# Kernel optimization log

Hardware: AMD Instinct MI355X
Metric: run time of the kernel (lower is better)

The kernel has to match this reference:

```python
import jax, jax.numpy as jnp
import numpy as np

B, T, D_MODEL = 2, 8192, 2048
H, H_KV, D_HEAD = 16, 8, 128
M_LAND, RANK = 64, 64
N_ITER = 6
STD = 0.02


def setup_inputs() -> dict:
    key = jax.random.key(0)
    ks = jax.random.split(key, 7)
    return {
        "x": jax.random.normal(ks[0], (B, T, D_MODEL), jnp.float32),
        "Wq": jax.random.normal(ks[1], (D_MODEL, H * D_HEAD), jnp.float32) * STD,
        "Wk": jax.random.normal(ks[2], (D_MODEL, H_KV * D_HEAD), jnp.float32) * STD,
        "Wv": jax.random.normal(ks[3], (D_MODEL, H_KV * D_HEAD), jnp.float32) * STD,
        "Wo": jax.random.normal(ks[4], (H * D_HEAD, D_MODEL), jnp.float32) * STD,
        "Wkp1": jax.random.normal(ks[5], (D_HEAD, RANK), jnp.float32) * STD,
        "Wkp2": jax.random.normal(ks[6], (RANK, D_HEAD), jnp.float32) * STD,
    }


def _iterative_pinv(A, n_iter=N_ITER):
    # A: (B, H, m, m); Schulz iteration Z <- 2Z - Z A Z
    norm_1 = jnp.max(jnp.sum(jnp.abs(A), axis=-2), axis=-1)
    norm_inf = jnp.max(jnp.sum(jnp.abs(A), axis=-1), axis=-1)
    v = 1.0 / jnp.clip(norm_1 * norm_inf, 1e-7)
    Z = jnp.swapaxes(A, -1, -2) * v[..., None, None]
    for _ in range(n_iter):
        Z = 2.0 * Z - Z @ A @ Z
    return Z


def reference(x, Wq, Wk, Wv, Wo, Wkp1, Wkp2):
    n_rep = H // H_KV
    # projections -> (B, H, T, d)
    q = (x @ Wq).reshape(B, T, H, D_HEAD).transpose(0, 2, 1, 3)
    k = (x @ Wk).reshape(B, T, H_KV, D_HEAD).transpose(0, 2, 1, 3)
    v = (x @ Wv).reshape(B, T, H_KV, D_HEAD).transpose(0, 2, 1, 3)
    k = jnp.repeat(k, n_rep, axis=1)  # GQA repeat_kv
    v = jnp.repeat(v, n_rep, axis=1)

    m = min(M_LAND, T)
    scale = 1.0 / np.sqrt(D_HEAD).astype(np.float32)
    stride = max(T // m, 1)
    idx = jnp.arange(0, T, stride)[:m]
    q_land = q[:, :, idx, :]
    k_land = k[:, :, idx, :]
    kernel_proj = lambda z: z + jax.nn.silu(z @ Wkp1) @ Wkp2
    q_land = kernel_proj(q_land)
    k_land = kernel_proj(k_land)

    K_qm = jax.nn.softmax(jnp.einsum('bhtd,bhmd->bhtm', q, k_land) * scale, axis=-1)
    K_mm = jax.nn.softmax(jnp.einsum('bhmd,bhnd->bhmn', q_land, k_land) * scale, axis=-1)
    K_mk = jax.nn.softmax(jnp.einsum('bhmd,bhtd->bhmt', q_land, k) * scale, axis=-1)
    K_mm_inv = _iterative_pinv(K_mm)

    # associativity-reordered (same math, avoids dense (T,T) intermediate)
    out = K_qm @ (K_mm_inv @ (K_mk @ v))  # (B, H, T, d)
    out = out.transpose(0, 2, 1, 3).reshape(B, T, H * D_HEAD)
    return out @ Wo
```

## Files before the change

### kernel.cpp

```cpp
#include <hip/hip_runtime.h>


#define B_ 2
#define T_ 8192
#define DM 2048
#define H_ 16
#define DH 128
#define NIT 6

typedef unsigned short u16;
typedef __attribute__((ext_vector_type(8))) short bf16x8;
typedef __attribute__((ext_vector_type(4))) float f32x4;
typedef __attribute__((ext_vector_type(4))) unsigned short u16x4;

__device__ __forceinline__ u16 f2bf(float f) {
    unsigned u = __float_as_uint(f);
    u += 0x7FFFu + ((u >> 16) & 1u);
    return (u16)(u >> 16);
}

__device__ __forceinline__ void async16(const void* g, void* l) {
    __builtin_amdgcn_global_load_lds((const __attribute__((address_space(1))) void*)g,
                                     (__attribute__((address_space(3))) void*)l,
                                     16, 0, 0);
}

__global__ void cvt_x_kernel(const float* __restrict__ x, u16* __restrict__ xb, int n4) {
    int i = blockIdx.x * blockDim.x + threadIdx.x;
    int stride = gridDim.x * blockDim.x;
    for (; i < n4; i += stride) {
        float4 v = ((const float4*)x)[i];
        u16x4 o;
        o.x = f2bf(v.x); o.y = f2bf(v.y); o.z = f2bf(v.z); o.w = f2bf(v.w);
        ((u16x4*)xb)[i] = o;
    }
}

__global__ void tconv_kernel(const float* __restrict__ src, u16* __restrict__ dst, int R, int C) {
    __shared__ float tl[32][33];
    int c0 = blockIdx.x * 32, r0 = blockIdx.y * 32;
    int tx = threadIdx.x, ty = threadIdx.y;
    #pragma unroll
    for (int i = ty; i < 32; i += 8)
        tl[i][tx] = src[(size_t)(r0 + i) * C + c0 + tx];
    __syncthreads();
    #pragma unroll
    for (int i = ty; i < 32; i += 8)
        dst[(size_t)(c0 + i) * R + r0 + tx] = f2bf(tl[tx][i]);
}

__global__ void tv_kernel(const u16* __restrict__ v, u16* __restrict__ vT) {
    int bg = blockIdx.z;
    const u16* src = v + (size_t)(bg >> 3) * T_ * 1024 + (bg & 7) * DH;
    u16* dst = vT + (size_t)bg * DH * T_;
    __shared__ u16 tl[32][33];
    int t0 = blockIdx.x * 32, d0 = blockIdx.y * 32;
    int tx = threadIdx.x, ty = threadIdx.y;
    #pragma unroll
    for (int i = ty; i < 32; i += 8)
        tl[i][tx] = src[(size_t)(t0 + i) * 1024 + d0 + tx];
    __syncthreads();
    #pragma unroll
    for (int i = ty; i < 32; i += 8)
        dst[(size_t)(d0 + i) * T_ + t0 + tx] = tl[tx][i];
}

template<int MODE>
__global__ __launch_bounds__(256) void gemm_bt_kernel(
    const u16* __restrict__ A, const u16* __restrict__ Bt,
    u16* __restrict__ oq, u16* __restrict__ ok, u16* __restrict__ ov,
    float* __restrict__ of, int M, int N, int K)
{
    __shared__ u16 la[128 * 32];
    __shared__ u16 lb[128 * 32];
    const int tid = threadIdx.x;
    const int lane = tid & 63;
    const int w = tid >> 6;
    const int wr = w >> 1, wc = w & 1;
    const int fr = lane & 15, fg = lane >> 4;
    const long row0 = (long)blockIdx.y * 128;
    const long col0 = (long)blockIdx.x * 128;

    const u16* ga = A + (row0 + (tid >> 2)) * (long)K + (tid & 3) * 8;
    const u16* gb = Bt + (col0 + (tid >> 2)) * (long)K + (tid & 3) * 8;
    char* la_b = (char*)la + w * 1024;
    char* lb_b = (char*)lb + w * 1024;

    const u16* lap = la + (wr * 64 + fr) * 32 + fg * 8;
    const u16* lbp = lb + (wc * 64 + fr) * 32 + fg * 8;

    f32x4 acc[4][4] = {};

    for (int k0 = 0; k0 < K; k0 += 32) {
        __syncthreads();
        async16(ga + k0, la_b);
        async16(ga + k0 + 64 * (long)K, la_b + 4096);
        async16(gb + k0, lb_b);
        async16(gb + k0 + 64 * (long)K, lb_b + 4096);
        __syncthreads();
        bf16x8 af[4], bfv[4];
        #pragma unroll
        for (int i = 0; i < 4; ++i) af[i] = *(const bf16x8*)(lap + i * 16 * 32);
        #pragma unroll
        for (int j = 0; j < 4; ++j) bfv[j] = *(const bf16x8*)(lbp + j * 16 * 32);
        #pragma unroll
        for (int i = 0; i < 4; ++i)
            #pragma unroll
            for (int j = 0; j < 4; ++j)
                acc[i][j] = __builtin_amdgcn_mfma_f32_16x16x32_bf16(af[i], bfv[j], acc[i][j], 0, 0, 0);
    }

    const long rbase = row0 + wr * 64 + fg * 4;
    const int nbase = (int)col0 + wc * 64 + fr;
    #pragma unroll
    for (int i = 0; i < 4; ++i)
        #pragma unroll
        for (int j = 0; j < 4; ++j)
            #pragma unroll
            for (int r = 0; r < 4; ++r) {
                long rg = rbase + i * 16 + r;
                int nn = nbase + j * 16;
                float val = acc[i][j][r];
                if (MODE == 0) {
                    u16 o = f2bf(val);
                    if (nn < 2048)      oq[rg * 2048 + nn] = o;
                    else if (nn < 3072) ok[rg * 1024 + (nn - 2048)] = o;
                    else                ov[rg * 1024 + (nn - 3072)] = o;
                } else {
                    of[rg * 2048 + nn] = val;
                }
            }
}

__global__ __launch_bounds__(256) void land_gemm_kernel(
    const float* __restrict__ x, const float* __restrict__ Wq,
    const float* __restrict__ Wk, float* __restrict__ land_raw)
{
    __shared__ float xs[128][36];
    __shared__ float ws[32][132];
    const int tid = threadIdx.x;
    const int n0 = blockIdx.x * 128;
    const int tm0 = (tid >> 4) * 8, tn0 = (tid & 15) * 8;
    float accr[8][8] = {};

    for (int it = 0; it < 8; ++it) {
        const int k0 = blockIdx.y * 256 + it * 32;
        __syncthreads();
        for (int idx = tid * 4; idx < 4096; idx += 1024) {
            int r = idx >> 5, c = idx & 31;
            *(float4*)&xs[r][c] =
                *(const float4*)&x[((size_t)(r >> 6) * T_ + (r & 63) * 128) * DM + k0 + c];
        }
        if (n0 < 2048) {
            for (int idx = tid * 4; idx < 4096; idx += 1024) {
                int k = idx >> 7, c = idx & 127;
                *(float4*)&ws[k][c] = *(const float4*)&Wq[(size_t)(k0 + k) * 2048 + n0 + c];
            }
        } else {
            for (int idx = tid * 4; idx < 4096; idx += 1024) {
                int k = idx >> 7, c = idx & 127;
                *(float4*)&ws[k][c] = *(const float4*)&Wk[(size_t)(k0 + k) * 1024 + (n0 - 2048) + c];
            }
        }
        __syncthreads();
        for (int k = 0; k < 32; ++k) {
            float a[8];
            #pragma unroll
            for (int i = 0; i < 8; ++i) a[i] = xs[tm0 + i][k];
            f32x4 b0 = *(const f32x4*)&ws[k][tn0];
            f32x4 b1 = *(const f32x4*)&ws[k][tn0 + 4];
            #pragma unroll
            for (int i = 0; i < 8; ++i) {
                accr[i][0] += a[i] * b0[0]; accr[i][1] += a[i] * b0[1];
                accr[i][2] += a[i] * b0[2]; accr[i][3] += a[i] * b0[3];
                accr[i][4] += a[i] * b1[0]; accr[i][5] += a[i] * b1[1];
                accr[i][6] += a[i] * b1[2]; accr[i][7] += a[i] * b1[3];
            }
        }
    }
    for (int i = 0; i < 8; ++i)
        for (int j = 0; j < 8; ++j)
            atomicAdd(&land_raw[(size_t)(tm0 + i) * 3072 + n0 + tn0 + j], accr[i][j]);
}

__global__ void proj_kernel(const float* __restrict__ land_raw,
    const float* __restrict__ Wkp1, const float* __restrict__ Wkp2,
    float* __restrict__ qlf, float* __restrict__ klf,
    u16* __restrict__ qlb, u16* __restrict__ klb)
{
    const int bid = blockIdx.x;
    const int type = bid & 1;
    const int m = (bid >> 1) & 63;
    const int bh = bid >> 7;
    const int b = bh >> 4, h = bh & 15;
    const int lane = threadIdx.x;
    const int lm = b * 64 + m;
    const float* src = (type == 0)
        ? land_raw + (size_t)lm * 3072 + h * 128
        : land_raw + (size_t)lm * 3072 + 2048 + (h >> 1) * 128;
    __shared__ float zb[128];
    __shared__ float sb[64];
    float z0 = src[lane], z1 = src[lane + 64];
    zb[lane] = z0; zb[lane + 64] = z1;
    __syncthreads();
    float hsum = 0.f;
    #pragma unroll 4
    for (int d = 0; d < 128; ++d) hsum += zb[d] * Wkp1[d * 64 + lane];
    sb[lane] = hsum / (1.f + __expf(-hsum));
    __syncthreads();
    float o0 = z0, o1 = z1;
    #pragma unroll 4
    for (int j = 0; j < 64; ++j) {
        float sj = sb[j];
        o0 += sj * Wkp2[j * 128 + lane];
        o1 += sj * Wkp2[j * 128 + lane + 64];
    }
    size_t oidx = ((size_t)bh * 64 + m) * 128 + lane;
    float* fo = (type == 0) ? qlf : klf;
    u16*   bo = (type == 0) ? qlb : klb;
    fo[oidx] = o0; fo[oidx + 64] = o1;
    bo[oidx] = f2bf(o0); bo[oidx + 64] = f2bf(o1);
}

__global__ __launch_bounds__(256) void pinv_kernel(
    const float* __restrict__ qlf, const float* __restrict__ klf, float* __restrict__ inv)
{
    const int bh = blockIdx.x;
    const int tid = threadIdx.x;
    const int m = tid >> 2, nq = tid & 3, n0b = nq * 16;
    __shared__ float Am[64][68];
    __shared__ float Z[64][68];
    __shared__ float Wm[64][68];
    __shared__ float cs[64], rsn[64];
    __shared__ float vsc;
    const float scale = 0.08838834764831845f;

    float accr[16] = {};
    const float* qrow = qlf + ((size_t)bh * 64 + m) * 128;
    for (int dc = 0; dc < 4; ++dc) {
        f32x4 qv[8];
        #pragma unroll
        for (int u = 0; u < 8; ++u) qv[u] = *(const f32x4*)&qrow[dc * 32 + u * 4];
        for (int nn = 0; nn < 16; ++nn) {
            const float* kp = klf + ((size_t)bh * 64 + n0b + nn) * 128 + dc * 32;
            float s = 0.f;
            #pragma unroll
            for (int u = 0; u < 8; ++u) {
                f32x4 kv = *(const f32x4*)&kp[u * 4];
                s += qv[u][0]*kv[0] + qv[u][1]*kv[1] + qv[u][2]*kv[2] + qv[u][3]*kv[3];
            }
            accr[nn] += s;
        }
    }
    float rsum = 0.f;
    #pragma unroll
    for (int nn = 0; nn < 16; ++nn) { accr[nn] = __expf(accr[nn] * scale); rsum += accr[nn]; }
    rsum += __shfl_xor(rsum, 1);
    rsum += __shfl_xor(rsum, 2);
    float rinv = 1.f / rsum;
    #pragma unroll
    for (int nn = 0; nn < 16; ++nn) Am[m][n0b + nn] = accr[nn] * rinv;
    __syncthreads();
    if (tid < 64) {
        float s = 0.f;
        for (int i = 0; i < 64; ++i) s += Am[i][tid];
        cs[tid] = s;
    } else if (tid < 128) {
        int r = tid - 64; float s = 0.f;
        for (int j = 0; j < 64; ++j) s += Am[r][j];
        rsn[r] = s;
    }
    __syncthreads();
    if (tid == 0) {
        float n1 = 0.f, ni = 0.f;
        for (int i = 0; i < 64; ++i) { n1 = fmaxf(n1, cs[i]); ni = fmaxf(ni, rsn[i]); }
        float pr = n1 * ni; if (pr < 1e-7f) pr = 1e-7f;
        vsc = 1.f / pr;
    }
    __syncthreads();
    {
        float v = vsc;
        for (int u = 0; u < 16; ++u) {
            int idx = tid * 16 + u;
            Z[idx >> 6][idx & 63] = Am[idx & 63][idx >> 6] * v;
        }
    }
    for (int it = 0; it < NIT; ++it) {
        __syncthreads();
        float wacc[16] = {};
        for (int k = 0; k < 64; ++k) {
            float a = Am[m][k];
            f32x4 z0 = *(const f32x4*)&Z[k][n0b];
            f32x4 z1 = *(const f32x4*)&Z[k][n0b + 4];
            f32x4 z2 = *(const f32x4*)&Z[k][n0b + 8];
            f32x4 z3 = *(const f32x4*)&Z[k][n0b + 12];
            #pragma unroll
            for (int u = 0; u < 4; ++u) {
                wacc[u]      += a * z0[u];
                wacc[u + 4]  += a * z1[u];
                wacc[u + 8]  += a * z2[u];
                wacc[u + 12] += a * z3[u];
            }
        }
        #pragma unroll
        for (int nn = 0; nn < 16; ++nn) Wm[m][n0b + nn] = wacc[nn];
        __syncthreads();
        float zacc[16] = {};
        for (int k = 0; k < 64; ++k) {
            float zk = Z[m][k];
            f32x4 w0 = *(const f32x4*)&Wm[k][n0b];
            f32x4 w1 = *(const f32x4*)&Wm[k][n0b + 4];
            f32x4 w2 = *(const f32x4*)&Wm[k][n0b + 8];
            f32x4 w3 = *(const f32x4*)&Wm[k][n0b + 12];
            #pragma unroll
            for (int u = 0; u < 4; ++u) {
                zacc[u]      += zk * w0[u];
                zacc[u + 4]  += zk * w1[u];
                zacc[u + 8]  += zk * w2[u];
                zacc[u + 12] += zk * w3[u];
            }
        }
        #pragma unroll
        for (int nn = 0; nn < 16; ++nn) zacc[nn] = 2.f * Z[m][n0b + nn] - zacc[nn];
        __syncthreads();
        #pragma unroll
        for (int nn = 0; nn < 16; ++nn) Z[m][n0b + nn] = zacc[nn];
    }
    __syncthreads();
    for (int u = 0; u < 16; ++u) {
        int idx = tid * 16 + u;
        inv[(size_t)bh * 4096 + idx] = Z[idx >> 6][idx & 63];
    }
}

__global__ __launch_bounds__(64) void attn_mk_kernel(
    const u16* __restrict__ qlb, const u16* __restrict__ kb,
    const u16* __restrict__ vT, float* __restrict__ agg_acc, float* __restrict__ agg_sum)
{
    const int bid = blockIdx.x;
    const int chunk = bid & 31;
    const int bh = bid >> 5;
    const int b = bh >> 4, h = bh & 15, g = h >> 1;
    const int t0 = chunk * 256;
    const int lane = threadIdx.x;
    const int fr = lane & 15, fg = lane >> 4;
    const float scale = 0.08838834764831845f;
    __shared__ u16 P[64][264];

    float rst[4][4] = {};
    const u16* qbase = qlb + ((size_t)bh * 64 + fr) * 128 + fg * 8;

    for (int sc = 0; sc < 4; ++sc) {
        f32x4 S[4][4] = {};
        const u16* kbase = kb + ((size_t)(b * T_ + t0 + sc * 64 + fr)) * 1024 + g * 128 + fg * 8;
        #pragma unroll
        for (int ks = 0; ks < 4; ++ks) {
            bf16x8 a[4], bv[4];
            #pragma unroll
            for (int i = 0; i < 4; ++i) a[i] = *(const bf16x8*)(qbase + (size_t)i * 16 * 128 + ks * 32);
            #pragma unroll
            for (int j = 0; j < 4; ++j) bv[j] = *(const bf16x8*)(kbase + (size_t)j * 16 * 1024 + ks * 32);
            #pragma unroll
            for (int i = 0; i < 4; ++i)
                #pragma unroll
                for (int j = 0; j < 4; ++j)
                    S[i][j] = __builtin_amdgcn_mfma_f32_16x16x32_bf16(a[i], bv[j], S[i][j], 0, 0, 0);
        }
        #pragma unroll
        for (int i = 0; i < 4; ++i)
            #pragma unroll
            for (int j = 0; j < 4; ++j)
                #pragma unroll
                for (int r = 0; r < 4; ++r) {
                    float pv = __expf(S[i][j][r] * scale);
                    rst[i][r] += pv;
                    P[i * 16 + fg * 4 + r][sc * 64 + j * 16 + fr] = f2bf(pv);
                }
    }
    __syncthreads();
    #pragma unroll
    for (int i = 0; i < 4; ++i)
        #pragma unroll
        for (int r = 0; r < 4; ++r) {
            float t = rst[i][r];
            t += __shfl_xor(t, 1); t += __shfl_xor(t, 2);
            t += __shfl_xor(t, 4); t += __shfl_xor(t, 8);
            if (fr == 0) atomicAdd(&agg_sum[(size_t)bh * 64 + i * 16 + fg * 4 + r], t);
        }
    const u16* vbase = vT + ((size_t)(b * 8 + g) * 128 + fr) * T_ + t0 + fg * 8;
    #pragma unroll
    for (int dh = 0; dh < 2; ++dh) {
        f32x4 O[4][4] = {};
        #pragma unroll
        for (int ks = 0; ks < 8; ++ks) {
            bf16x8 pa[4], vv[4];
            #pragma unroll
            for (int i = 0; i < 4; ++i) pa[i] = *(const bf16x8*)&P[i * 16 + fr][ks * 32 + fg * 8];
            #pragma unroll
            for (int j = 0; j < 4; ++j) vv[j] = *(const bf16x8*)(vbase + ((size_t)dh * 64 + j * 16) * T_ + ks * 32);
            #pragma unroll
            for (int i = 0; i < 4; ++i)
                #pragma unroll
                for (int j = 0; j < 4; ++j)
                    O[i][j] = __builtin_amdgcn_mfma_f32_16x16x32_bf16(pa[i], vv[j], O[i][j], 0, 0, 0);
        }
        #pragma unroll
        for (int i = 0; i < 4; ++i)
            #pragma unroll
            for (int j = 0; j < 4; ++j)
                #pragma unroll
                for (int r = 0; r < 4; ++r)
                    atomicAdd(&agg_acc[((size_t)bh * 64 + i * 16 + fg * 4 + r) * 128 + dh * 64 + j * 16 + fr],
                              O[i][j][r]);
    }
}

__global__ __launch_bounds__(256) void mid_kernel(
    const float* __restrict__ inv, const float* __restrict__ agg_acc,
    const float* __restrict__ agg_sum, u16* __restrict__ midt)
{
    const int bh = blockIdx.x;
    const int tid = threadIdx.x;
    __shared__ float invl[64][68];
    __shared__ float an[64][129];
    for (int idx = tid; idx < 4096; idx += 256)
        invl[idx >> 6][idx & 63] = inv[(size_t)bh * 4096 + idx];
    for (int idx = tid; idx < 8192; idx += 256) {
        int j = idx >> 7, d = idx & 127;
        an[j][d] = agg_acc[((size_t)bh * 64 + j) * 128 + d] / agg_sum[(size_t)bh * 64 + j];
    }
    __syncthreads();
    const int m = tid >> 2, dq = tid & 3;
    float accv[32] = {};
    for (int j = 0; j < 64; ++j) {
        float a = invl[m][j];
        #pragma unroll
        for (int dd = 0; dd < 32; ++dd)
            accv[dd] += a * an[j][dq * 32 + dd];
    }
    for (int dd = 0; dd < 32; ++dd)
        midt[(size_t)bh * 8192 + (dq * 32 + dd) * 64 + m] = f2bf(accv[dd]);
}

__global__ __launch_bounds__(256) void attn_qm_kernel(
    const u16* __restrict__ qb, const u16* __restrict__ klb,
    const u16* __restrict__ midt, u16* __restrict__ ao)
{
    const int bid = blockIdx.x;
    const int tile = bid & 63;
    const int bh = bid >> 6;
    const int b = bh >> 4, h = bh & 15;
    const int w = threadIdx.x >> 6;
    const int lane = threadIdx.x & 63;
    const int fr = lane & 15, fg = lane >> 4;
    const int trow0 = tile * 128 + w * 32;
    const float scale = 0.08838834764831845f;
    __shared__ u16 Pl[4][32][72];

    f32x4 S[2][4] = {};
    const u16* qbase = qb + ((size_t)(b * T_ + trow0 + fr)) * 2048 + h * 128 + fg * 8;
    const u16* kbase = klb + ((size_t)bh * 64 + fr) * 128 + fg * 8;
    #pragma unroll
    for (int ks = 0; ks < 4; ++ks) {
        bf16x8 a[2], bv[4];
        #pragma unroll
        for (int i = 0; i < 2; ++i) a[i] = *(const bf16x8*)(qbase + (size_t)i * 16 * 2048 + ks * 32);
        #pragma unroll
        for (int j = 0; j < 4; ++j) bv[j] = *(const bf16x8*)(kbase + (size_t)j * 16 * 128 + ks * 32);
        #pragma unroll
        for (int i = 0; i < 2; ++i)
            #pragma unroll
            for (int j = 0; j < 4; ++j)
                S[i][j] = __builtin_amdgcn_mfma_f32_16x16x32_bf16(a[i], bv[j], S[i][j], 0, 0, 0);
    }
    #pragma unroll
    for (int i = 0; i < 2; ++i) {
        float rsv[4] = {0.f, 0.f, 0.f, 0.f};
        #pragma unroll
        for (int j = 0; j < 4; ++j)
            #pragma unroll
            for (int r = 0; r < 4; ++r) {
                float pv = __expf(S[i][j][r] * scale);
                S[i][j][r] = pv;
                rsv[r] += pv;
            }
        #pragma unroll
        for (int r = 0; r < 4; ++r) {
            float t = rsv[r];
            t += __shfl_xor(t, 1); t += __shfl_xor(t, 2);
            t += __shfl_xor(t, 4); t += __shfl_xor(t, 8);
            rsv[r] = 1.f / t;
        }
        #pragma unroll
        for (int j = 0; j < 4; ++j)
            #pragma unroll
            for (int r = 0; r < 4; ++r)
                Pl[w][i * 16 + fg * 4 + r][j * 16 + fr] = f2bf(S[i][j][r] * rsv[r]);
    }
    __syncthreads();
    f32x4 O[2][8] = {};
    const u16* mbase = midt + ((size_t)bh * 128 + fr) * 64 + fg * 8;
    #pragma unroll
    for (int ks = 0; ks < 2; ++ks) {
        bf16x8 pa[2], mb[8];
        #pragma unroll
        for (int i = 0; i < 2; ++i) pa[i] = *(const bf16x8*)&Pl[w][i * 16 + fr][ks * 32 + fg * 8];
        #pragma unroll
        for (int j = 0; j < 8; ++j) mb[j] = *(const bf16x8*)(mbase + (size_t)j * 16 * 64 + ks * 32);
        #pragma unroll
        for (int i = 0; i < 2; ++i)
            #pragma unroll
            for (int j = 0; j < 8; ++j)
                O[i][j] = __builtin_amdgcn_mfma_f32_16x16x32_bf16(pa[i], mb[j], O[i][j], 0, 0, 0);
    }
    u16* obase = ao + ((size_t)(b * T_ + trow0 + fg * 4)) * 2048 + h * 128 + fr;
    #pragma unroll
    for (int i = 0; i < 2; ++i)
        #pragma unroll
        for (int j = 0; j < 8; ++j)
            #pragma unroll
            for (int r = 0; r < 4; ++r)
                obase[((size_t)i * 16 + r) * 2048 + j * 16] = f2bf(O[i][j][r]);
}

extern "C" void kernel_launch(void* const* d_in, const int* in_sizes, int n_in,
                              void* d_out, int out_size, void* d_ws, size_t ws_size,
                              hipStream_t stream)
{
    const float* x    = (const float*)d_in[0];
    const float* Wq   = (const float*)d_in[1];
    const float* Wk   = (const float*)d_in[2];
    const float* Wv   = (const float*)d_in[3];
    const float* Wo   = (const float*)d_in[4];
    const float* Wkp1 = (const float*)d_in[5];
    const float* Wkp2 = (const float*)d_in[6];
    float* out = (float*)d_out;

    char* p = (char*)d_ws;
    auto alloc = [&](size_t bytes) { char* r = p; p += (bytes + 255) & ~(size_t)255; return r; };
    u16*   x_bf     = (u16*)alloc(67108864);
    u16*   q_bf     = (u16*)alloc(67108864);
    u16*   kv_bf    = (u16*)alloc(67108864);
    u16*   Wcat_t   = (u16*)alloc(16777216);
    float* land_raw = (float*)alloc(1572864);
    float* qlf      = (float*)alloc(2097152);
    float* klf      = (float*)alloc(2097152);
    u16*   qlb      = (u16*)alloc(1048576);
    u16*   klb      = (u16*)alloc(1048576);
    float* invb     = (float*)alloc(524288);
    float* agg_acc  = (float*)alloc(2097152);
    float* agg_sum  = (float*)alloc(32768);
    u16*   midt     = (u16*)alloc(1048576);

    u16* k_bf = kv_bf;
    u16* v_bf = kv_bf + (size_t)16384 * 1024;
    u16* vT       = x_bf;
    u16* attn_out = kv_bf;
    u16* Wo_t     = Wcat_t;

    (void)hipMemsetAsync(land_raw, 0, 1572864, stream);
    (void)hipMemsetAsync(agg_acc, 0, 2097152, stream);
    (void)hipMemsetAsync(agg_sum, 0, 32768, stream);

    cvt_x_kernel<<<2048, 256, 0, stream>>>(x, x_bf, 16384 * 2048 / 4);
    tconv_kernel<<<dim3(64, 64), dim3(32, 8), 0, stream>>>(Wq, Wcat_t, 2048, 2048);
    tconv_kernel<<<dim3(32, 64), dim3(32, 8), 0, stream>>>(Wk, Wcat_t + (size_t)2048 * 2048, 2048, 1024);
    tconv_kernel<<<dim3(32, 64), dim3(32, 8), 0, stream>>>(Wv, Wcat_t + (size_t)3072 * 2048, 2048, 1024);
    gemm_bt_kernel<0><<<dim3(32, 128), 256, 0, stream>>>(x_bf, Wcat_t, q_bf, k_bf, v_bf, nullptr,
                                                         16384, 4096, 2048);
    land_gemm_kernel<<<dim3(24, 8), 256, 0, stream>>>(x, Wq, Wk, land_raw);
    proj_kernel<<<4096, 64, 0, stream>>>(land_raw, Wkp1, Wkp2, qlf, klf, qlb, klb);
    pinv_kernel<<<32, 256, 0, stream>>>(qlf, klf, invb);
    tv_kernel<<<dim3(256, 4, 16), dim3(32, 8), 0, stream>>>(v_bf, vT);
    attn_mk_kernel<<<1024, 64, 0, stream>>>(qlb, k_bf, vT, agg_acc, agg_sum);
    mid_kernel<<<32, 256, 0, stream>>>(invb, agg_acc, agg_sum, midt);
    tconv_kernel<<<dim3(64, 64), dim3(32, 8), 0, stream>>>(Wo, Wo_t, 2048, 2048);
    attn_qm_kernel<<<2048, 256, 0, stream>>>(q_bf, klb, midt, attn_out);
    gemm_bt_kernel<1><<<dim3(16, 128), 256, 0, stream>>>(attn_out, Wo_t, nullptr, nullptr, nullptr, out,
                                                         16384, 2048, 2048);
}
```

Baseline: 1.252 ms.

## Replace projection GEMMs with 256x256 double-buffered swizzled pipelined MFMA kernel

New measurement: 1.084 ms. 1.16x faster.

```diff
diff --git a/kernel.cpp b/kernel.cpp
--- a/kernel.cpp
+++ b/kernel.cpp
@@ -65,62 +65,139 @@
         dst[(size_t)(d0 + i) * T_ + t0 + tx] = tl[tx][i];
 }
 
+
+#define BAR()   __builtin_amdgcn_s_barrier()
+#define SB0()   __builtin_amdgcn_sched_barrier(0)
+#define LGKM0() do { asm volatile("s_waitcnt lgkmcnt(0)" ::: "memory"); SB0(); } while (0)
+#define VM6()   do { asm volatile("s_waitcnt vmcnt(6)" ::: "memory"); } while (0)
+
+#define RD_A(S, BUF, H) do {                                                  \
+    const char* _p = lA_rd + (BUF) * 32768 + (H) * 16384;                     \
+    _Pragma("unroll") for (int _m = 0; _m < 4; ++_m) {                        \
+        Af[S][_m][0] = *(const bf16x8*)(_p + _m * 2048 + kswz0);              \
+        Af[S][_m][1] = *(const bf16x8*)(_p + _m * 2048 + kswz1);              \
+    }                                                                         \
+} while (0)
+
+#define RD_B(S, BUF, H) do {                                                  \
+    const char* _p = lB_rd + (BUF) * 32768 + (H) * 16384;                     \
+    _Pragma("unroll") for (int _n = 0; _n < 2; ++_n) {                        \
+        Bf[S][_n][0] = *(const bf16x8*)(_p + _n * 2048 + kswz0);              \
+        Bf[S][_n][1] = *(const bf16x8*)(_p + _n * 2048 + kswz1);              \
+    }                                                                         \
+} while (0)
+
+#define ST_A(BUF, H, T) do {                                                  \
+    const u16* _g = gA + (size_t)(H) * 64 * K + (size_t)(T) * 64;             \
+    char* _l = lsAst + (BUF) * 32768 + (H) * 16384;                           \
+    async16(_g, _l);                                                          \
+    async16(_g + (size_t)128 * K, _l + 8192);                                 \
+} while (0)
+
+#define ST_B(BUF, H, T) do {                                                  \
+    const u16* _g = gB + (size_t)(H) * 32 * K + (size_t)(T) * 64;             \
+    char* _l = lsBst + (BUF) * 32768 + (H) * 16384;                           \
+    async16(_g, _l);                                                          \
+    async16(_g + (size_t)128 * K, _l + 8192);                                 \
+} while (0)
+
+#define MFMA_Q(AM, BN)                                                        \
+    _Pragma("unroll") for (int _m = 0; _m < 4; ++_m)                          \
+    _Pragma("unroll") for (int _n = 0; _n < 2; ++_n)                          \
+    _Pragma("unroll") for (int _k = 0; _k < 2; ++_k)                          \
+        acc[(AM) * 4 + _m][(BN) * 2 + _n] =                                   \
+            __builtin_amdgcn_mfma_f32_16x16x32_bf16(                          \
+                Af[AM][_m][_k], Bf[BN][_n][_k],                               \
+                acc[(AM) * 4 + _m][(BN) * 2 + _n], 0, 0, 0);
+
 template<int MODE>
-__global__ __launch_bounds__(256) void gemm_bt_kernel(
+__global__ __launch_bounds__(512) void gemm256_kernel(
     const u16* __restrict__ A, const u16* __restrict__ Bt,
     u16* __restrict__ oq, u16* __restrict__ ok, u16* __restrict__ ov,
-    float* __restrict__ of, int M, int N, int K)
-{
-    __shared__ u16 la[128 * 32];
-    __shared__ u16 lb[128 * 32];
-    const int tid = threadIdx.x;
+    float* __restrict__ of, int K, int nxt)
+{
+    __shared__ u16 lsA[2][2][128][64];
+    __shared__ u16 lsB[2][2][128][64];
+
+    const int tid  = threadIdx.x;
     const int lane = tid & 63;
-    const int w = tid >> 6;
-    const int wr = w >> 1, wc = w & 1;
-    const int fr = lane & 15, fg = lane >> 4;
-    const long row0 = (long)blockIdx.y * 128;
-    const long col0 = (long)blockIdx.x * 128;
-
-    const u16* ga = A + (row0 + (tid >> 2)) * (long)K + (tid & 3) * 8;
-    const u16* gb = Bt + (col0 + (tid >> 2)) * (long)K + (tid & 3) * 8;
-    char* la_b = (char*)la + w * 1024;
-    char* lb_b = (char*)lb + w * 1024;
-
-    const u16* lap = la + (wr * 64 + fr) * 32 + fg * 8;
-    const u16* lbp = lb + (wc * 64 + fr) * 32 + fg * 8;
-
-    f32x4 acc[4][4] = {};
-
-    for (int k0 = 0; k0 < K; k0 += 32) {
-        __syncthreads();
-        async16(ga + k0, la_b);
-        async16(ga + k0 + 64 * (long)K, la_b + 4096);
-        async16(gb + k0, lb_b);
-        async16(gb + k0 + 64 * (long)K, lb_b + 4096);
-        __syncthreads();
-        bf16x8 af[4], bfv[4];
-        #pragma unroll
-        for (int i = 0; i < 4; ++i) af[i] = *(const bf16x8*)(lap + i * 16 * 32);
-        #pragma unroll
-        for (int j = 0; j < 4; ++j) bfv[j] = *(const bf16x8*)(lbp + j * 16 * 32);
-        #pragma unroll
-        for (int i = 0; i < 4; ++i)
-            #pragma unroll
-            for (int j = 0; j < 4; ++j)
-                acc[i][j] = __builtin_amdgcn_mfma_f32_16x16x32_bf16(af[i], bfv[j], acc[i][j], 0, 0, 0);
-    }
-
-    const long rbase = row0 + wr * 64 + fg * 4;
-    const int nbase = (int)col0 + wc * 64 + fr;
-    #pragma unroll
-    for (int i = 0; i < 4; ++i)
-        #pragma unroll
-        for (int j = 0; j < 4; ++j)
-            #pragma unroll
-            for (int r = 0; r < 4; ++r) {
-                long rg = rbase + i * 16 + r;
-                int nn = nbase + j * 16;
-                float val = acc[i][j][r];
+    const int w    = tid >> 6;
+    const int wr   = w >> 2, wc = w & 3;
+    const int fr   = lane & 15, fg = lane >> 4;
+
+    const int cpx = (int)gridDim.x >> 3;
+    const int bid = ((int)blockIdx.x & 7) * cpx + ((int)blockIdx.x >> 3);
+    const int bx = bid % nxt, by = bid / nxt;
+    const long R0 = (long)by * 256, C0 = (long)bx * 256;
+
+    const int sr = tid >> 3;
+    const int sc = tid & 7;
+    const int koff = ((sc ^ (sr & 7)) * 8);
+    const u16* gA = A  + (R0 + sr) * (size_t)K + koff;
+    const u16* gB = Bt + (C0 + (sr >> 5) * 64 + (sr & 31)) * (size_t)K + koff;
+    char* lsAst = (char*)lsA + w * 1024;
+    char* lsBst = (char*)lsB + w * 1024;
+
+    const int kswz0 = (0 * 64 + fg * 16) ^ ((fr & 7) << 4);
+    const int kswz1 = (1 * 64 + fg * 16) ^ ((fr & 7) << 4);
+    const char* lA_rd = (const char*)lsA + (wr * 64 + fr) * 128;
+    const char* lB_rd = (const char*)lsB + (wc * 32 + fr) * 128;
+
+    f32x4 acc[8][4] = {};
+    bf16x8 Af[2][4][2], Bf[2][2][2];
+
+    const int NT = K >> 6;
+
+    ST_A(0, 0, 0); ST_B(0, 0, 0); ST_B(0, 1, 0); ST_A(0, 1, 0);
+    ST_A(1, 0, 1); ST_B(1, 0, 1); ST_B(1, 1, 1);
+    VM6();
+    BAR(); SB0();
+
+    for (int t = 0; t < NT; ++t) {
+        const int buf = t & 1;
+        RD_A(0, buf, 0);
+        if (t + 1 < NT) ST_A(buf ^ 1, 1, t + 1);
+        BAR(); LGKM0();
+        __builtin_amdgcn_s_setprio(1);
+        if (t > 0) { MFMA_Q(1, 1); }
+        __builtin_amdgcn_s_setprio(0);
+        BAR(); SB0();
+        RD_B(0, buf, 0);
+        if (t + 2 < NT) ST_A(buf, 0, t + 2);
+        BAR(); LGKM0();
+        __builtin_amdgcn_s_setprio(1);
+        MFMA_Q(0, 0);
+        __builtin_amdgcn_s_setprio(0);
+        BAR(); SB0();
+        RD_B(1, buf, 1);
+        if (t + 2 < NT) ST_B(buf, 0, t + 2);
+        BAR(); LGKM0();
+        __builtin_amdgcn_s_setprio(1);
+        MFMA_Q(0, 1);
+        __builtin_amdgcn_s_setprio(0);
+        BAR(); SB0();
+        RD_A(1, buf, 1);
+        if (t + 2 < NT) ST_B(buf, 1, t + 2);
+        VM6();
+        BAR(); LGKM0();
+        __builtin_amdgcn_s_setprio(1);
+        MFMA_Q(1, 0);
+        __builtin_amdgcn_s_setprio(0);
+        BAR(); SB0();
+    }
+    MFMA_Q(1, 1);
+
+    const long rb0 = R0 + wr * 128 + fg * 4;
+    const int  cb0 = (int)C0 + wc * 64 + fr;
+    #pragma unroll
+    for (int mi = 0; mi < 8; ++mi)
+        #pragma unroll
+        for (int ni = 0; ni < 4; ++ni)
+            #pragma unroll
+            for (int rr = 0; rr < 4; ++rr) {
+                long rg = rb0 + mi * 16 + rr;
+                int  nn = cb0 + ni * 16;
+                float val = acc[mi][ni][rr];
                 if (MODE == 0) {
                     u16 o = f2bf(val);
                     if (nn < 2048)      oq[rg * 2048 + nn] = o;
@@ -566,8 +643,7 @@
     tconv_kernel<<<dim3(64, 64), dim3(32, 8), 0, stream>>>(Wq, Wcat_t, 2048, 2048);
     tconv_kernel<<<dim3(32, 64), dim3(32, 8), 0, stream>>>(Wk, Wcat_t + (size_t)2048 * 2048, 2048, 1024);
     tconv_kernel<<<dim3(32, 64), dim3(32, 8), 0, stream>>>(Wv, Wcat_t + (size_t)3072 * 2048, 2048, 1024);
-    gemm_bt_kernel<0><<<dim3(32, 128), 256, 0, stream>>>(x_bf, Wcat_t, q_bf, k_bf, v_bf, nullptr,
-                                                         16384, 4096, 2048);
+    gemm256_kernel<0><<<1024, 512, 0, stream>>>(x_bf, Wcat_t, q_bf, k_bf, v_bf, nullptr, 2048, 16);
     land_gemm_kernel<<<dim3(24, 8), 256, 0, stream>>>(x, Wq, Wk, land_raw);
     proj_kernel<<<4096, 64, 0, stream>>>(land_raw, Wkp1, Wkp2, qlf, klf, qlb, klb);
     pinv_kernel<<<32, 256, 0, stream>>>(qlf, klf, invb);
@@ -576,6 +652,5 @@
     mid_kernel<<<32, 256, 0, stream>>>(invb, agg_acc, agg_sum, midt);
     tconv_kernel<<<dim3(64, 64), dim3(32, 8), 0, stream>>>(Wo, Wo_t, 2048, 2048);
     attn_qm_kernel<<<2048, 256, 0, stream>>>(q_bf, klb, midt, attn_out);
-    gemm_bt_kernel<1><<<dim3(16, 128), 256, 0, stream>>>(attn_out, Wo_t, nullptr, nullptr, nullptr, out,
-                                                         16384, 2048, 2048);
-}
+    gemm256_kernel<1><<<512, 512, 0, stream>>>(attn_out, Wo_t, nullptr, nullptr, nullptr, out, 2048, 8);
+}
```
